# Optimization experiments

Hardware: AMD Instinct MI355X
Metric: run time of the kernel (lower is better)

## Reference

```python
import jax, jax.numpy as jnp
import numpy as np

N = 16384
IMRATIO = 0.0732
MARGIN = 1.0


def setup_inputs() -> dict:
    key = jax.random.key(0)
    k1, k2 = jax.random.split(key)
    preds = jax.random.normal(k1, (N,), dtype=jnp.float32)
    targets = (jax.random.uniform(k2, (N,)) < IMRATIO).astype(jnp.int32)
    return {"preds": preds, "targets": targets}


def reference(preds, targets):
    # positive = preds[targets==1]; negative = preds[targets==0]
    # loss = mean over P x N pairs of (1 - (p_i - n_j))**2 + margin * relu(1 - (p_i - n_j))
    # Expressed jit-compatibly as a mask-weighted full pairwise reduction (same math).
    pos_w = (targets == 1).astype(preds.dtype)  # [N]
    neg_w = (targets == 0).astype(preds.dtype)  # [N]
    one_minus_diff = 1.0 - (preds[:, None] - preds[None, :])  # [N, N]
    vals = one_minus_diff * one_minus_diff + MARGIN * jax.nn.relu(one_minus_diff)
    w = pos_w[:, None] * neg_w[None, :]  # [N, N] pair indicator
    num_pairs = pos_w.sum() * neg_w.sum()
    return (vals * w).sum() / num_pairs
```

## Files before the change

kernel.cpp:

```cpp
#include <hip/hip_runtime.h>


#define TILE  1024
#define NTIL  16
#define NJB   64

__device__ __forceinline__ double wave_reduce_f64(double v) {
    #pragma unroll
    for (int off = 32; off > 0; off >>= 1) v += __shfl_xor(v, off, 64);
    return v;
}

__global__ __launch_bounds__(256)
void aucm_pair(const float* __restrict__ preds,
               const int* __restrict__ tgt,
               int n,
               double* __restrict__ reluPart,
               double* __restrict__ momPart)
{
    __shared__ __align__(16) float sP[TILE];
    __shared__ int sWaveC[4];
    __shared__ double sRed[4][6];

    const int tid  = threadIdx.x;
    const int lane = tid & 63;
    const int wave = tid >> 6;
    const int b    = blockIdx.x;
    const int jb   = b & (NJB - 1);
    const int it   = b >> 6;
    const bool doMom = (jb == 0);

    const int base = it * TILE + (tid << 2);
    const int4   t4 = *reinterpret_cast<const int4*>(&tgt[base]);
    const float4 p4 = *reinterpret_cast<const float4*>(&preds[base]);
    const int f0 = (t4.x == 1), f1 = (t4.y == 1),
              f2 = (t4.z == 1), f3 = (t4.w == 1);
    const int c = f0 + f1 + f2 + f3;

    int v = c;
    #pragma unroll
    for (int d = 1; d < 64; d <<= 1) {
        const int t = __shfl_up(v, d, 64);
        if (lane >= d) v += t;
    }
    if (lane == 63) sWaveC[wave] = v;
    __syncthreads();
    int wOff = 0;
    #pragma unroll
    for (int w = 0; w < 4; ++w) if (w < wave) wOff += sWaveC[w];
    const int cntP = sWaveC[0] + sWaveC[1] + sWaveC[2] + sWaveC[3];

    int g = wOff + v - c;
    if (f0) sP[g++] = 1.0f - p4.x;
    if (f1) sP[g++] = 1.0f - p4.y;
    if (f2) sP[g++] = 1.0f - p4.z;
    if (f3) sP[g++] = 1.0f - p4.w;

    double mA = 0, mA2 = 0, mN = 0, mN2 = 0;
    if (doMom) {
        const float pv[4] = { p4.x, p4.y, p4.z, p4.w };
        const int   fv[4] = { f0, f1, f2, f3 };
        #pragma unroll
        for (int u = 0; u < 4; ++u) {
            if (fv[u]) { const double a = 1.0 - (double)pv[u]; mA += a; mA2 += a * a; }
            else       { const double p = (double)pv[u];       mN += p; mN2 += p * p; }
        }
    }
    __syncthreads();

    const int j = (jb << 8) + tid;
    double accd = 0.0;
    if (tgt[j] == 0) {
        const float pj = preds[j];
        int k = 0;
        while (k < cntP) {
            const int end = min(cntP, k + 64);
            float a0 = 0.f, a1 = 0.f;
            for (; k + 8 <= end; k += 8) {
                const float4 v0 = *reinterpret_cast<const float4*>(&sP[k]);
                const float4 v1 = *reinterpret_cast<const float4*>(&sP[k + 4]);
                a0 += fmaxf(v0.x + pj, 0.f);
                a1 += fmaxf(v0.y + pj, 0.f);
                a0 += fmaxf(v0.z + pj, 0.f);
                a1 += fmaxf(v0.w + pj, 0.f);
                a0 += fmaxf(v1.x + pj, 0.f);
                a1 += fmaxf(v1.y + pj, 0.f);
                a0 += fmaxf(v1.z + pj, 0.f);
                a1 += fmaxf(v1.w + pj, 0.f);
            }
            float at = a0 + a1;
            for (; k < end; ++k) at += fmaxf(sP[k] + pj, 0.f);
            accd += (double)at;
        }
    }

    double r = wave_reduce_f64(accd);
    if (lane == 0) sRed[wave][0] = r;
    if (doMom) {
        const double rA  = wave_reduce_f64(mA);
        const double rA2 = wave_reduce_f64(mA2);
        const double rN  = wave_reduce_f64(mN);
        const double rN2 = wave_reduce_f64(mN2);
        if (lane == 0) {
            sRed[wave][1] = rA; sRed[wave][2] = rA2;
            sRed[wave][3] = rN; sRed[wave][4] = rN2;
        }
    }
    __syncthreads();
    if (tid == 0) {
        reluPart[b] = sRed[0][0] + sRed[1][0] + sRed[2][0] + sRed[3][0];
        if (doMom) {
            double tA = 0, tA2 = 0, tN = 0, tN2 = 0;
            #pragma unroll
            for (int w = 0; w < 4; ++w) {
                tA += sRed[w][1]; tA2 += sRed[w][2];
                tN += sRed[w][3]; tN2 += sRed[w][4];
            }
            momPart[it * 8 + 0] = tA;  momPart[it * 8 + 1] = tA2;
            momPart[it * 8 + 2] = tN;  momPart[it * 8 + 3] = tN2;
            momPart[it * 8 + 4] = (double)cntP;
        }
    }
}

__global__ __launch_bounds__(256)
void aucm_fin(const double* __restrict__ reluPart,
              const double* __restrict__ momPart,
              int n, float* __restrict__ out, float margin)
{
    __shared__ double sRedR[4];
    const int tid  = threadIdx.x;
    const int lane = tid & 63;
    const int wave = tid >> 6;

    double r = reluPart[tid] + reluPart[tid + 256]
             + reluPart[tid + 512] + reluPart[tid + 768];
    r = wave_reduce_f64(r);
    if (lane == 0) sRedR[wave] = r;

    double mA = 0, mA2 = 0, mN = 0, mN2 = 0, pc = 0;
    if (tid < NTIL) {
        mA  = momPart[tid * 8 + 0]; mA2 = momPart[tid * 8 + 1];
        mN  = momPart[tid * 8 + 2]; mN2 = momPart[tid * 8 + 3];
        pc  = momPart[tid * 8 + 4];
    }
    if (wave == 0) {
        mA  = wave_reduce_f64(mA);  mA2 = wave_reduce_f64(mA2);
        mN  = wave_reduce_f64(mN);  mN2 = wave_reduce_f64(mN2);
        pc  = wave_reduce_f64(pc);
    }
    __syncthreads();
    if (tid == 0) {
        const double tR = sRedR[0] + sRedR[1] + sRedR[2] + sRedR[3];
        const double P  = pc;
        const double Nn = (double)n - P;
        const double sq = Nn * mA2 + 2.0 * mA * mN + P * mN2;
        out[0] = (float)((sq + (double)margin * tR) / (P * Nn));
    }
}

extern "C" void kernel_launch(void* const* d_in, const int* in_sizes, int n_in,
                              void* d_out, int out_size, void* d_ws, size_t ws_size,
                              hipStream_t stream) {
    const float* preds = (const float*)d_in[0];
    const int*   tgt   = (const int*)d_in[1];
    float* out = (float*)d_out;
    const int n = in_sizes[0];

    char* ws = (char*)d_ws;
    double* reluPart = (double*)(ws + 0);
    double* momPart  = (double*)(ws + 8192);

    aucm_pair<<<NJB * NTIL, 256, 0, stream>>>(preds, tgt, n, reluPart, momPart);
    aucm_fin<<<1, 256, 0, stream>>>(reluPart, momPart, n, out, 1.0f );
}
```

Measured before the change: 62.93 us.

## Process two negative columns per thread to reuse LDS positive loads

Each thread now handles two j indices, so every LDS read of a positive value feeds two relu accumulations, and the grid shrinks to half as many blocks. The per-thread branch on the target label is replaced by computing both columns unconditionally and zeroing afterwards, which removes divergence but spends work on positive columns. The per-block positive-compaction prologue is amortised over twice as much work, though fewer blocks may reduce occupancy across CUs.

```diff
diff --git a/kernel.cpp b/kernel.cpp
--- a/kernel.cpp
+++ b/kernel.cpp
@@ -3,7 +3,8 @@
 
 #define TILE  1024
 #define NTIL  16
-#define NJB   64
+#define NJB   32
+#define NBLK  (NJB * NTIL)
 
 __device__ __forceinline__ double wave_reduce_f64(double v) {
     #pragma unroll
@@ -27,12 +28,19 @@
     const int wave = tid >> 6;
     const int b    = blockIdx.x;
     const int jb   = b & (NJB - 1);
-    const int it   = b >> 6;
+    const int it   = b >> 5;
     const bool doMom = (jb == 0);
 
     const int base = it * TILE + (tid << 2);
     const int4   t4 = *reinterpret_cast<const int4*>(&tgt[base]);
     const float4 p4 = *reinterpret_cast<const float4*>(&preds[base]);
+    const int j0 = (jb << 9) + tid;
+    const int j1 = j0 + 256;
+    const int   tj0 = tgt[j0];
+    const int   tj1 = tgt[j1];
+    const float pj0 = preds[j0];
+    const float pj1 = preds[j1];
+
     const int f0 = (t4.x == 1), f1 = (t4.y == 1),
               f2 = (t4.z == 1), f3 = (t4.w == 1);
     const int c = f0 + f1 + f2 + f3;
@@ -68,33 +76,39 @@
     }
     __syncthreads();
 
-    const int j = (jb << 8) + tid;
-    double accd = 0.0;
-    if (tgt[j] == 0) {
-        const float pj = preds[j];
+    double accd0 = 0.0, accd1 = 0.0;
+    {
         int k = 0;
         while (k < cntP) {
             const int end = min(cntP, k + 64);
             float a0 = 0.f, a1 = 0.f;
+            float b0 = 0.f, b1 = 0.f;
             for (; k + 8 <= end; k += 8) {
                 const float4 v0 = *reinterpret_cast<const float4*>(&sP[k]);
                 const float4 v1 = *reinterpret_cast<const float4*>(&sP[k + 4]);
-                a0 += fmaxf(v0.x + pj, 0.f);
-                a1 += fmaxf(v0.y + pj, 0.f);
-                a0 += fmaxf(v0.z + pj, 0.f);
-                a1 += fmaxf(v0.w + pj, 0.f);
-                a0 += fmaxf(v1.x + pj, 0.f);
-                a1 += fmaxf(v1.y + pj, 0.f);
-                a0 += fmaxf(v1.z + pj, 0.f);
-                a1 += fmaxf(v1.w + pj, 0.f);
+                a0 += fmaxf(v0.x + pj0, 0.f);  b0 += fmaxf(v0.x + pj1, 0.f);
+                a1 += fmaxf(v0.y + pj0, 0.f);  b1 += fmaxf(v0.y + pj1, 0.f);
+                a0 += fmaxf(v0.z + pj0, 0.f);  b0 += fmaxf(v0.z + pj1, 0.f);
+                a1 += fmaxf(v0.w + pj0, 0.f);  b1 += fmaxf(v0.w + pj1, 0.f);
+                a0 += fmaxf(v1.x + pj0, 0.f);  b0 += fmaxf(v1.x + pj1, 0.f);
+                a1 += fmaxf(v1.y + pj0, 0.f);  b1 += fmaxf(v1.y + pj1, 0.f);
+                a0 += fmaxf(v1.z + pj0, 0.f);  b0 += fmaxf(v1.z + pj1, 0.f);
+                a1 += fmaxf(v1.w + pj0, 0.f);  b1 += fmaxf(v1.w + pj1, 0.f);
             }
-            float at = a0 + a1;
-            for (; k < end; ++k) at += fmaxf(sP[k] + pj, 0.f);
-            accd += (double)at;
+            float at = a0 + a1, bt = b0 + b1;
+            for (; k < end; ++k) {
+                const float s = sP[k];
+                at += fmaxf(s + pj0, 0.f);
+                bt += fmaxf(s + pj1, 0.f);
+            }
+            accd0 += (double)at;
+            accd1 += (double)bt;
         }
     }
+    if (tj0 != 0) accd0 = 0.0;
+    if (tj1 != 0) accd1 = 0.0;
 
-    double r = wave_reduce_f64(accd);
+    double r = wave_reduce_f64(accd0 + accd1);
     if (lane == 0) sRed[wave][0] = r;
     if (doMom) {
         const double rA  = wave_reduce_f64(mA);
@@ -133,8 +147,7 @@
     const int lane = tid & 63;
     const int wave = tid >> 6;
 
-    double r = reluPart[tid] + reluPart[tid + 256]
-             + reluPart[tid + 512] + reluPart[tid + 768];
+    double r = reluPart[tid] + reluPart[tid + 256];
     r = wave_reduce_f64(r);
     if (lane == 0) sRedR[wave] = r;
 
@@ -169,8 +182,8 @@
 
     char* ws = (char*)d_ws;
     double* reluPart = (double*)(ws + 0);
-    double* momPart  = (double*)(ws + 8192);
+    double* momPart  = (double*)(ws + 4096);
 
-    aucm_pair<<<NJB * NTIL, 256, 0, stream>>>(preds, tgt, n, reluPart, momPart);
+    aucm_pair<<<NBLK, 256, 0, stream>>>(preds, tgt, n, reluPart, momPart);
     aucm_fin<<<1, 256, 0, stream>>>(reluPart, momPart, n, out, 1.0f );
 }
```

New measurement: 61.16 us. 2.8% less time.
